# Kernel tuning notes

Hardware: AMD Instinct MI355X
Metric: run time of the kernel (lower is better)

The kernel has to match this reference:

```python
import jax, jax.numpy as jnp
import numpy as np

HEADS = 8
D_MODEL = 512

def setup_inputs() -> dict:
    key = jax.random.key(0)
    ks = jax.random.split(key, 7)
    t, w, h, b = 8, 14, 14, 8
    seq = t * w * h + 1  # 1569, includes CLS token
    q = jax.random.normal(ks[0], (seq, b, D_MODEL), jnp.float32)
    k = jax.random.normal(ks[1], (seq, b, D_MODEL), jnp.float32)
    value = jax.random.normal(ks[2], (seq, b, D_MODEL), jnp.float32)
    in_proj_weight = jax.random.normal(ks[3], (3 * D_MODEL, D_MODEL), jnp.float32) * (D_MODEL ** -0.5)
    in_proj_bias = jax.random.normal(ks[4], (3 * D_MODEL,), jnp.float32) * 0.02
    out_w = jax.random.normal(ks[5], (D_MODEL, D_MODEL), jnp.float32) * (D_MODEL ** -0.5)
    out_b = jax.random.normal(ks[6], (D_MODEL,), jnp.float32) * 0.02
    return {"q": q, "k": k, "value": value,
            "in_proj_weight": in_proj_weight, "in_proj_bias": in_proj_bias,
            "out_w": out_w, "out_b": out_b, "t": t, "w": w, "h": h}

def _sdpa(q, k, v):
    # scaled dot-product attention over batched 3D tensors [B, L, dh]
    temp = q.shape[-1] ** 0.5
    scores = jnp.einsum('bqd,bkd->bqk', q, k) / temp
    a = jax.nn.softmax(scores, axis=-1)  # softmax over dim=2 == last dim
    return jnp.einsum('bqk,bkd->bqd', a, v), a

def reference(q, k, value, in_proj_weight, in_proj_bias, out_w, out_b, t, w, h):
    seq, b, c = q.shape
    H, dh, wh = HEADS, c // HEADS, w * h
    q_cls = q[:1]          # [1, b, c] passed through untouched
    x = q[1:]              # [t*wh, b, c]
    qkv = x @ in_proj_weight.T + in_proj_bias  # fused QKV proj
    qq, kk, vv = qkv[..., :c], qkv[..., c:2 * c], qkv[..., 2 * c:]
    to5 = lambda z: z.reshape(t, wh, b, H, dh)
    # spatial stage: batch = (H, b, t), attend over wh
    q_s = to5(qq).transpose(3, 2, 0, 1, 4).reshape(H * b * t, wh, dh)
    k_s = to5(kk).transpose(3, 2, 0, 1, 4).reshape(H * b * t, wh, dh)
    v_s = to5(vv).transpose(3, 2, 0, 1, 4).reshape(H * b * t, wh, dh)
    out_s, attn = _sdpa(q_s, k_s, v_s)
    # temporal stage: batch = (H, b, wh), attend over t; V comes from spatial output
    v_t = out_s.reshape(H, b, t, wh, dh).transpose(0, 1, 3, 2, 4).reshape(H * b * wh, t, dh)
    q_t = to5(qq).transpose(3, 2, 1, 0, 4).reshape(H * b * wh, t, dh)
    k_t = to5(kk).transpose(3, 2, 1, 0, 4).reshape(H * b * wh, t, dh)
    out_t, _ = _sdpa(q_t, k_t, v_t)
    # back to [t*wh, b, c]
    out = out_t.reshape(H, b, wh, t, dh).transpose(3, 2, 1, 0, 4).reshape(t * wh, b, c)
    out = out @ out_w.T + out_b
    return jnp.concatenate([q_cls, out], axis=0), attn
```

## Files before the change

### kernel.cpp

```cpp
#include <hip/hip_runtime.h>
#include <cstdint>
#include <cstddef>

typedef __bf16 bf16;
typedef __bf16 bf16x8 __attribute__((ext_vector_type(8)));
typedef __bf16 bf16x4 __attribute__((ext_vector_type(4)));
typedef float  f32x4  __attribute__((ext_vector_type(4)));

#define MFMA16(a, b, c) __builtin_amdgcn_mfma_f32_16x16x32_bf16(a, b, c, 0, 0, 0)

__device__ __forceinline__ void gl2lds16(const bf16* g, bf16* l) {
  __builtin_amdgcn_global_load_lds(
      (const __attribute__((address_space(1))) void*)g,
      (__attribute__((address_space(3))) void*)l, 16, 0, 0);
}

__device__ __forceinline__ void cvt4(const float* __restrict__ s, bf16* __restrict__ d) {
  f32x4 v = *(const f32x4*)s;
  bf16x4 o;
  o[0] = (bf16)v[0]; o[1] = (bf16)v[1]; o[2] = (bf16)v[2]; o[3] = (bf16)v[3];
  *(bf16x4*)d = o;
}

__global__ __launch_bounds__(256) void prep_kernel(
    const float* __restrict__ q, const float* __restrict__ win,
    const float* __restrict__ wout, float* __restrict__ out0,
    bf16* __restrict__ xb, bf16* __restrict__ wqb, bf16* __restrict__ wob) {
  long u = (long)blockIdx.x * 256 + threadIdx.x;
  const long NX4 = 1605632, NWQ4 = 196608, NWO4 = 65536, NQC4 = 1024;
  if (u < NX4) { cvt4(q + 4096 + u * 4, xb + u * 4); return; }
  u -= NX4;
  if (u < NWQ4) { cvt4(win + u * 4, wqb + u * 4); return; }
  u -= NWQ4;
  if (u < NWO4) { cvt4(wout + u * 4, wob + u * 4); return; }
  u -= NWO4;
  if (u < NQC4) { *(f32x4*)(out0 + u * 4) = *(const f32x4*)(q + u * 4); }
}

__global__ __launch_bounds__(256) void gemm_bt(
    const bf16* __restrict__ A, const bf16* __restrict__ Bm,
    const float* __restrict__ bias, float* __restrict__ Cf,
    int N, int K, long coff) {
  __shared__ bf16 As[128 * 64];
  __shared__ bf16 Bs[128 * 64];
  const int tid = threadIdx.x;
  const int wid = tid >> 6, lane = tid & 63;
  const int lr = lane & 15, lg = lane >> 4;

  const int nwg = gridDim.x * gridDim.y;
  const int orig = blockIdx.y * gridDim.x + blockIdx.x;
  const int cpx = nwg >> 3;
  const int swz = (orig & 7) * cpx + (orig >> 3);
  const int m0 = (swz / gridDim.x) * 128;
  const int n0 = (swz % gridDim.x) * 128;

  const int wr = wid >> 1, wc = wid & 1;
  const int slot = lane & 7, r8 = lane >> 3;
  const int chunk = slot ^ r8;
  const int x7 = lr & 7;

  f32x4 acc[4][4] = {};

  for (int kt = 0; kt < K; kt += 64) {
    __syncthreads();
#pragma unroll
    for (int j = 0; j < 4; ++j) {
      int blk = wid * 4 + j;
      int row = blk * 8 + r8;
      gl2lds16(A + (size_t)(m0 + row) * K + kt + chunk * 8, As + blk * 512);
      gl2lds16(Bm + (size_t)(n0 + row) * K + kt + chunk * 8, Bs + blk * 512);
    }
    __syncthreads();

#pragma unroll
    for (int kk = 0; kk < 2; ++kk) {
      bf16x8 af[4], bfr[4];
#pragma unroll
      for (int m = 0; m < 4; ++m)
        af[m] = *(const bf16x8*)(As + (wr * 64 + m * 16 + lr) * 64 +
                                 (((kk * 4 + lg) ^ x7) * 8));
#pragma unroll
      for (int n = 0; n < 4; ++n)
        bfr[n] = *(const bf16x8*)(Bs + (wc * 64 + n * 16 + lr) * 64 +
                                  (((kk * 4 + lg) ^ x7) * 8));
#pragma unroll
      for (int m = 0; m < 4; ++m)
#pragma unroll
        for (int n = 0; n < 4; ++n)
          acc[m][n] = MFMA16(af[m], bfr[n], acc[m][n]);
    }
  }

#pragma unroll
  for (int m = 0; m < 4; ++m) {
    int row = m0 + wr * 64 + m * 16 + lg * 4;
#pragma unroll
    for (int n = 0; n < 4; ++n) {
      int col = n0 + wc * 64 + n * 16 + lr;
      float bv = bias[col];
#pragma unroll
      for (int i = 0; i < 4; ++i)
        __builtin_nontemporal_store(
            acc[m][n][i] + bv, Cf + coff + (size_t)(row + i) * N + col);
    }
  }
}

__global__ __launch_bounds__(1024) void spatial_fused(
    const bf16* __restrict__ xb, const bf16* __restrict__ wqb,
    const float* __restrict__ bin, bf16* __restrict__ Qh,
    bf16* __restrict__ Kh, float* __restrict__ attn_out,
    bf16* __restrict__ outs) {
  __shared__ bf16 Kl[224 * 72];
  __shared__ bf16 Vt[64 * 232];
  __shared__ bf16 RB[40768];
  bf16* const Xs  = RB;
  bf16* const Wss = RB + 13312;
  bf16* const Qb  = RB + 25600;
  bf16* const StgB = RB;

  const int tid = threadIdx.x;
  const int wid = tid >> 6, lane = tid & 63;
  const int lr = lane & 15, lg = lane >> 4;
  const int batch = blockIdx.x;
  const int h = batch >> 6;
  const int bb = (batch >> 3) & 7;
  const int ti = batch & 7;

  { int d = tid >> 4, r = 208 + (tid & 15); Vt[d * 232 + r] = (bf16)0.f; }

  const int r8 = lane >> 3, slot = lane & 7;
  const int chunk = slot ^ r8;
  const int qt = wid;
  const int x7 = lr & 7;

  f32x4 acc[12] = {};

  for (int kt = 0; kt < 512; kt += 64) {
    __syncthreads();
#pragma unroll
    for (int t = 0; t < 4; ++t) {
      int task = wid + t * 16;
      if (task < 26) {
        int row = task * 8 + r8;
        int xr = row > 195 ? 195 : row;
        gl2lds16(xb + ((size_t)(ti * 196 + xr) * 8 + bb) * 512 + kt +
                     chunk * 8,
                 Xs + task * 512);
      } else if (task < 50) {
        int j = task - 26;
        int strip = j >> 3;
        int wrow = strip * 512 + h * 64 + (j & 7) * 8 + r8;
        gl2lds16(wqb + (size_t)wrow * 512 + kt + chunk * 8, Wss + j * 512);
      }
    }
    __syncthreads();
    if (qt < 13) {
#pragma unroll
      for (int kk = 0; kk < 2; ++kk) {
        bf16x8 af = *(const bf16x8*)(Xs + (qt * 16 + lr) * 64 +
                                     (((kk * 4 + lg) ^ x7) * 8));
#pragma unroll
        for (int nf = 0; nf < 12; ++nf) {
          bf16x8 bfr = *(const bf16x8*)(Wss + (nf * 16 + lr) * 64 +
                                        (((kk * 4 + lg) ^ x7) * 8));
          acc[nf] = MFMA16(af, bfr, acc[nf]);
        }
      }
    }
  }

  bf16x8 aq[2];
  if (qt < 13) {
#pragma unroll
    for (int nf = 0; nf < 12; ++nf) {
      int strip = nf >> 2;
      float bv = bin[strip * 512 + h * 64 + (nf & 3) * 16 + lr];
#pragma unroll
      for (int i = 0; i < 4; ++i) acc[nf][i] += bv;
    }
    bf16* qb = Qb + qt * 1152;
#pragma unroll
    for (int nf = 0; nf < 4; ++nf)
#pragma unroll
      for (int i = 0; i < 4; ++i)
        qb[(lg * 4 + i) * 72 + nf * 16 + lr] = (bf16)acc[nf][i];
#pragma unroll
    for (int nf = 4; nf < 8; ++nf)
#pragma unroll
      for (int i = 0; i < 4; ++i)
        Kl[(qt * 16 + lg * 4 + i) * 72 + (nf - 4) * 16 + lr] =
            (bf16)acc[nf][i];
#pragma unroll
    for (int nf = 8; nf < 12; ++nf) {
      union { bf16x4 h4; uint2 u; } pk;
      pk.h4[0] = (bf16)acc[nf][0]; pk.h4[1] = (bf16)acc[nf][1];
      pk.h4[2] = (bf16)acc[nf][2]; pk.h4[3] = (bf16)acc[nf][3];
      int d = (nf - 8) * 16 + lr;
      *(uint2*)&Vt[d * 232 + qt * 16 + lg * 4] = pk.u;
    }
#pragma unroll
    for (int kk = 0; kk < 2; ++kk)
      aq[kk] = *(const bf16x8*)(qb + lr * 72 + kk * 32 + lg * 8);
    {
      bf16* slabQ = Qh + (size_t)batch * 12544;
      bf16* slabK = Kh + (size_t)batch * 12544;
      const int erow = lane >> 3, eseg = lane & 7;
#pragma unroll
      for (int t = 0; t < 2; ++t) {
        int row = qt * 16 + t * 8 + erow;
        if (row < 196) {
          bf16x8 qv = *(const bf16x8*)(qb + (t * 8 + erow) * 72 + eseg * 8);
          *(bf16x8*)(slabQ + row * 64 + eseg * 8) = qv;
          bf16x8 kv = *(const bf16x8*)(Kl + row * 72 + eseg * 8);
          *(bf16x8*)(slabK + row * 64 + eseg * 8) = kv;
        }
      }
    }
  }
  __syncthreads();

  if (qt < 13) {
    const int q = qt * 16 + lr;

    f32x4 s[14] = {};
    __builtin_amdgcn_s_setprio(1);
#pragma unroll
    for (int nn = 0; nn < 14; ++nn) {
      const int krow = nn * 16 + lr;
      bf16x8 bk0 = *(const bf16x8*)&Kl[krow * 72 + lg * 8];
      bf16x8 bk1 = *(const bf16x8*)&Kl[krow * 72 + 32 + lg * 8];
      s[nn] = MFMA16(bk0, aq[0], s[nn]);
      s[nn] = MFMA16(bk1, aq[1], s[nn]);
    }
    __builtin_amdgcn_s_setprio(0);

#pragma unroll
    for (int nn = 0; nn < 14; ++nn) {
      bool pad = (nn * 16 + lg * 4 >= 196);
#pragma unroll
      for (int i = 0; i < 4; ++i)
        s[nn][i] = pad ? -1e30f : s[nn][i] * 0.125f;
    }

    float v = -1e30f;
#pragma unroll
    for (int nn = 0; nn < 14; ++nn)
#pragma unroll
      for (int i = 0; i < 4; ++i) v = fmaxf(v, s[nn][i]);
    v = fmaxf(v, __shfl_xor(v, 16));
    v = fmaxf(v, __shfl_xor(v, 32));
    float sum = 0.f;
#pragma unroll
    for (int nn = 0; nn < 14; ++nn)
#pragma unroll
      for (int i = 0; i < 4; ++i) {
        float e = __expf(s[nn][i] - v);
        s[nn][i] = e;
        sum += e;
      }
    sum += __shfl_xor(sum, 16);
    sum += __shfl_xor(sum, 32);
    const float rinv = 1.f / sum;

    bf16* const tile = StgB + qt * 3136;
    const int low = lr + 32 * (lg & 1);
    const int high = low + 16;
    const bool hiN = (lg >> 1) != 0;
    f32x4 o[4] = {};
#pragma unroll
    for (int kb = 0; kb < 7; ++kb) {
      uint32_t px[2], py[2];
#pragma unroll
      for (int t = 0; t < 2; ++t) {
        const int nn = 2 * kb + t;
        f32x4 sv;
#pragma unroll
        for (int i = 0; i < 4; ++i) sv[i] = s[nn][i] * rinv;
        union { bf16x4 h4; uint2 u; } pk;
        pk.h4[0] = (bf16)sv[0]; pk.h4[1] = (bf16)sv[1];
        pk.h4[2] = (bf16)sv[2]; pk.h4[3] = (bf16)sv[3];
        int kbase = nn * 16 + lg * 4;
        if (kbase < 196)
          *(uint2*)((char*)tile + lr * 392 + kbase * 2) = pk.u;
        px[t] = pk.u.x; py[t] = pk.u.y;
      }
      uint32_t a0x = __shfl((int)px[0], low);
      uint32_t a0y = __shfl((int)py[0], low);
      uint32_t a1x = __shfl((int)px[1], low);
      uint32_t a1y = __shfl((int)py[1], low);
      uint32_t b0x = __shfl((int)px[0], high);
      uint32_t b0y = __shfl((int)py[0], high);
      uint32_t b1x = __shfl((int)px[1], high);
      uint32_t b1y = __shfl((int)py[1], high);
      union { uint32_t u[4]; bf16x8 h8; } pa;
      pa.u[0] = hiN ? a1x : a0x;
      pa.u[1] = hiN ? a1y : a0y;
      pa.u[2] = hiN ? b1x : b0x;
      pa.u[3] = hiN ? b1y : b0y;
      __builtin_amdgcn_s_setprio(1);
#pragma unroll
      for (int nd = 0; nd < 4; ++nd) {
        bf16x8 vb = *(const bf16x8*)&Vt[(nd * 16 + lr) * 232 + kb * 32 + lg * 8];
        o[nd] = MFMA16(pa.h8, vb, o[nd]);
      }
      __builtin_amdgcn_s_setprio(0);
    }

    {
      const int hb8 = batch >> 3;
#pragma unroll
      for (int i = 0; i < 4; ++i) {
        int p = qt * 16 + lg * 4 + i;
        if (p < 196) {
#pragma unroll
          for (int nd = 0; nd < 4; ++nd) {
            int d = nd * 16 + lr;
            outs[(((size_t)(hb8 * 196 + p)) * 8 + ti) * 64 + d] =
                (bf16)o[nd][i];
          }
        }
      }
    }

    {
      const int vbytes = (qt == 12) ? 3136 : 12544;
      char* dst = (char*)(attn_out + (size_t)batch * 38416 + qt * 3136);
      const char* src = (const char*)tile;
#pragma unroll
      for (int j = 0; j < 13; ++j) {
        int x = j * 1024 + lane * 16;
        if (x < vbytes) {
          uint2 u = *(const uint2*)(src + (x >> 1));
          union { uint32_t b; float f; } c0, c1, c2, c3;
          c0.b = (u.x & 0xffffu) << 16; c1.b = u.x & 0xffff0000u;
          c2.b = (u.y & 0xffffu) << 16; c3.b = u.y & 0xffff0000u;
          f32x4 ov; ov[0] = c0.f; ov[1] = c1.f; ov[2] = c2.f; ov[3] = c3.f;
          *(f32x4*)(dst + x) = ov;
        }
      }
    }
  }
}

__global__ __launch_bounds__(256) void temporal_attn(
    const bf16* __restrict__ Qh, const bf16* __restrict__ Kh,
    const bf16* __restrict__ outs, bf16* __restrict__ outt) {
  __shared__ bf16 Ql[4][8][72];
  __shared__ bf16 Kc[4][8][72];
  __shared__ bf16 Vl[4][8][64];
  __shared__ float Ps[4][8][8];

  const int tid = threadIdx.x, wid = tid >> 6, lane = tid & 63;
  const int batch = blockIdx.x * 4 + wid;
  const int p = batch % 196;
  const int hb = batch / 196;
  const int bb = hb & 7, h = hb >> 3;

  const int ri = lane >> 3;
  const int c8 = lane & 7;
  {
    size_t so = ((size_t)(h * 64 + bb * 8 + ri)) * 12544 + p * 64 + c8 * 8;
    *(bf16x8*)&Ql[wid][ri][c8 * 8] = *(const bf16x8*)(Qh + so);
    *(bf16x8*)&Kc[wid][ri][c8 * 8] = *(const bf16x8*)(Kh + so);
    *(bf16x8*)&Vl[wid][ri][c8 * 8] =
        *(const bf16x8*)(outs + ((size_t)batch * 8 + ri) * 64 + c8 * 8);
  }
  __syncthreads();

  float s = 0.f;
#pragma unroll
  for (int d = 0; d < 64; d += 8) {
    bf16x8 qv = *(const bf16x8*)&Ql[wid][ri][d];
    bf16x8 kv = *(const bf16x8*)&Kc[wid][c8][d];
#pragma unroll
    for (int e = 0; e < 8; ++e) s += (float)qv[e] * (float)kv[e];
  }
  s *= 0.125f;
  float mxv = s;
#pragma unroll
  for (int d2 = 1; d2 < 8; d2 <<= 1) mxv = fmaxf(mxv, __shfl_xor(mxv, d2));
  float e = __expf(s - mxv);
  float sum = e;
#pragma unroll
  for (int d2 = 1; d2 < 8; d2 <<= 1) sum += __shfl_xor(sum, d2);
  Ps[wid][ri][c8] = e / sum;
  __syncthreads();

  const int d = lane;
#pragma unroll
  for (int ii = 0; ii < 8; ++ii) {
    float o = 0.f;
#pragma unroll
    for (int j = 0; j < 8; ++j) o += Ps[wid][ii][j] * (float)Vl[wid][j][d];
    outt[((size_t)(ii * 196 + p) * 8 + bb) * 512 + h * 64 + d] = (bf16)o;
  }
}

extern "C" void kernel_launch(void* const* d_in, const int* in_sizes, int n_in,
                              void* d_out, int out_size, void* d_ws,
                              size_t ws_size, hipStream_t stream) {
  (void)in_sizes; (void)n_in; (void)out_size; (void)ws_size;
  const float* q    = (const float*)d_in[0];
  const float* win  = (const float*)d_in[3];
  const float* bin  = (const float*)d_in[4];
  const float* wout = (const float*)d_in[5];
  const float* bout = (const float*)d_in[6];
  float* out0 = (float*)d_out;
  float* attn = out0 + 6426624L;

  bf16* Qh   = (bf16*)d_ws;
  bf16* Kh   = Qh + 6422528L;
  bf16* outs = Kh + 6422528L;
  bf16* outt = outs + 6422528L;
  bf16* wob  = outt + 6422528L;
  bf16* xb   = wob + 262144L;

  bf16* wqb = (bf16*)(out0 + 4096);

  prep_kernel<<<7300, 256, 0, stream>>>(q, win, wout, out0, xb, wqb, wob);
  spatial_fused<<<512, 1024, 0, stream>>>(xb, wqb, bin, Qh, Kh, attn, outs);
  temporal_attn<<<3136, 256, 0, stream>>>(Qh, Kh, outs, outt);
  gemm_bt<<<dim3(4, 98), 256, 0, stream>>>(outt, wob, bout, out0, 512, 512,
                                           4096);
}
```

Baseline: 92.27 us.

## Retile fused QKV projection across all 16 waves as 4x3 fragment blocks

Replaces the QKV projection work split, where 13 of 16 waves each computed a 16-row tile across all 12 output fragments, with a 4x4 wave grid. Each wave now computes 4 row tiles by 3 column fragments. This uses all waves and reuses each A and B fragment load across several MFMAs, cutting LDS reads per MFMA. It adds an extra block barrier before the attention phase, because Q/K/V tiles in LDS are now written by different waves, and it computes padded row tiles beyond 13.

```diff
diff --git a/kernel.cpp b/kernel.cpp
--- a/kernel.cpp
+++ b/kernel.cpp
@@ -131,10 +131,11 @@
 
   const int r8 = lane >> 3, slot = lane & 7;
   const int chunk = slot ^ r8;
-  const int qt = wid;
   const int x7 = lr & 7;
 
-  f32x4 acc[12] = {};
+  const int qg = wid >> 2, ng = wid & 3;
+  const int nfb = ng * 3;
+  f32x4 acc[4][3] = {};
 
   for (int kt = 0; kt < 512; kt += 64) {
     __syncthreads();
@@ -155,66 +156,75 @@
       }
     }
     __syncthreads();
-    if (qt < 13) {
-#pragma unroll
-      for (int kk = 0; kk < 2; ++kk) {
-        bf16x8 af = *(const bf16x8*)(Xs + (qt * 16 + lr) * 64 +
-                                     (((kk * 4 + lg) ^ x7) * 8));
-#pragma unroll
-        for (int nf = 0; nf < 12; ++nf) {
-          bf16x8 bfr = *(const bf16x8*)(Wss + (nf * 16 + lr) * 64 +
-                                        (((kk * 4 + lg) ^ x7) * 8));
-          acc[nf] = MFMA16(af, bfr, acc[nf]);
+#pragma unroll
+    for (int kk = 0; kk < 2; ++kk) {
+      const int xoff = ((kk * 4 + lg) ^ x7) * 8;
+      bf16x8 af[4];
+#pragma unroll
+      for (int qi = 0; qi < 4; ++qi)
+        af[qi] = *(const bf16x8*)(Xs + ((qg * 4 + qi) * 16 + lr) * 64 + xoff);
+#pragma unroll
+      for (int nj = 0; nj < 3; ++nj) {
+        bf16x8 bfr = *(const bf16x8*)(Wss + ((nfb + nj) * 16 + lr) * 64 + xoff);
+#pragma unroll
+        for (int qi = 0; qi < 4; ++qi)
+          acc[qi][nj] = MFMA16(af[qi], bfr, acc[qi][nj]);
+      }
+    }
+  }
+
+#pragma unroll
+  for (int qi = 0; qi < 4; ++qi) {
+    const int qtg = qg * 4 + qi;
+    if (qtg < 13) {
+#pragma unroll
+      for (int nj = 0; nj < 3; ++nj) {
+        const int nf = nfb + nj;
+        const int strip = nf >> 2;
+        float bv = bin[strip * 512 + h * 64 + (nf & 3) * 16 + lr];
+        f32x4 a = acc[qi][nj];
+#pragma unroll
+        for (int i = 0; i < 4; ++i) a[i] += bv;
+        if (strip == 0) {
+          bf16* qb = Qb + qtg * 1152;
+#pragma unroll
+          for (int i = 0; i < 4; ++i)
+            qb[(lg * 4 + i) * 72 + (nf & 3) * 16 + lr] = (bf16)a[i];
+        } else if (strip == 1) {
+#pragma unroll
+          for (int i = 0; i < 4; ++i)
+            Kl[(qtg * 16 + lg * 4 + i) * 72 + (nf & 3) * 16 + lr] =
+                (bf16)a[i];
+        } else {
+          union { bf16x4 h4; uint2 u; } pk;
+          pk.h4[0] = (bf16)a[0]; pk.h4[1] = (bf16)a[1];
+          pk.h4[2] = (bf16)a[2]; pk.h4[3] = (bf16)a[3];
+          int d = (nf & 3) * 16 + lr;
+          *(uint2*)&Vt[d * 232 + qtg * 16 + lg * 4] = pk.u;
         }
       }
     }
   }
-
+  __syncthreads();
+
+  const int qt = wid;
   bf16x8 aq[2];
   if (qt < 13) {
-#pragma unroll
-    for (int nf = 0; nf < 12; ++nf) {
-      int strip = nf >> 2;
-      float bv = bin[strip * 512 + h * 64 + (nf & 3) * 16 + lr];
-#pragma unroll
-      for (int i = 0; i < 4; ++i) acc[nf][i] += bv;
-    }
-    bf16* qb = Qb + qt * 1152;
-#pragma unroll
-    for (int nf = 0; nf < 4; ++nf)
-#pragma unroll
-      for (int i = 0; i < 4; ++i)
-        qb[(lg * 4 + i) * 72 + nf * 16 + lr] = (bf16)acc[nf][i];
-#pragma unroll
-    for (int nf = 4; nf < 8; ++nf)
-#pragma unroll
-      for (int i = 0; i < 4; ++i)
-        Kl[(qt * 16 + lg * 4 + i) * 72 + (nf - 4) * 16 + lr] =
-            (bf16)acc[nf][i];
-#pragma unroll
-    for (int nf = 8; nf < 12; ++nf) {
-      union { bf16x4 h4; uint2 u; } pk;
-      pk.h4[0] = (bf16)acc[nf][0]; pk.h4[1] = (bf16)acc[nf][1];
-      pk.h4[2] = (bf16)acc[nf][2]; pk.h4[3] = (bf16)acc[nf][3];
-      int d = (nf - 8) * 16 + lr;
-      *(uint2*)&Vt[d * 232 + qt * 16 + lg * 4] = pk.u;
-    }
+    const bf16* qb = Qb + qt * 1152;
 #pragma unroll
     for (int kk = 0; kk < 2; ++kk)
       aq[kk] = *(const bf16x8*)(qb + lr * 72 + kk * 32 + lg * 8);
-    {
-      bf16* slabQ = Qh + (size_t)batch * 12544;
-      bf16* slabK = Kh + (size_t)batch * 12544;
-      const int erow = lane >> 3, eseg = lane & 7;
-#pragma unroll
-      for (int t = 0; t < 2; ++t) {
-        int row = qt * 16 + t * 8 + erow;
-        if (row < 196) {
-          bf16x8 qv = *(const bf16x8*)(qb + (t * 8 + erow) * 72 + eseg * 8);
-          *(bf16x8*)(slabQ + row * 64 + eseg * 8) = qv;
-          bf16x8 kv = *(const bf16x8*)(Kl + row * 72 + eseg * 8);
-          *(bf16x8*)(slabK + row * 64 + eseg * 8) = kv;
-        }
+    bf16* slabQ = Qh + (size_t)batch * 12544;
+    bf16* slabK = Kh + (size_t)batch * 12544;
+    const int erow = lane >> 3, eseg = lane & 7;
+#pragma unroll
+    for (int t = 0; t < 2; ++t) {
+      int row = qt * 16 + t * 8 + erow;
+      if (row < 196) {
+        *(bf16x8*)(slabQ + row * 64 + eseg * 8) =
+            *(const bf16x8*)(qb + (t * 8 + erow) * 72 + eseg * 8);
+        *(bf16x8*)(slabK + row * 64 + eseg * 8) =
+            *(const bf16x8*)(Kl + row * 72 + eseg * 8);
       }
     }
   }
```

Result: faster. 89.50 us, median of 2 (-3.0%).
